# Optimization experiments

Hardware: AMD Instinct MI355X
Metric: run time of the kernel (lower is better)

Reference implementation:

```python
import jax, jax.numpy as jnp
import numpy as np

B, G, D, H, KD, E = 64, 512, 128, 8, 16, 128
NS = 20  # num_station


def _init_w(key, shape):
    stdv = 1.0 / np.sqrt(shape[-1]).astype(np.float32)
    return jax.random.uniform(key, shape, jnp.float32, -stdv, stdv)


def setup_inputs() -> dict:
    key = jax.random.key(0)
    ks = jax.random.split(key, 12)
    return {
        "q": jax.random.normal(ks[0], (B, G, D), jnp.float32),
        "h": jax.random.normal(ks[1], (B, G, D), jnp.float32),
        "W_query_depot": _init_w(ks[2], (H, D, KD)),
        "W_key_custom": _init_w(ks[3], (H, D, KD)),
        "W_val_custom": _init_w(ks[4], (H, D, KD)),
        "W_query_station": _init_w(ks[5], (H, D, KD)),
        "W_key_other": _init_w(ks[6], (H, D, KD)),
        "W_val_other": _init_w(ks[7], (H, D, KD)),
        "W_query_custom": _init_w(ks[8], (H, D, KD)),
        "W_key_all": _init_w(ks[9], (H, D, KD)),
        "W_val_all": _init_w(ks[10], (H, D, KD)),
        "W_out": _init_w(ks[11], (H, KD, E)),
        "num_station": NS,
    }


def _mha_block(q_seg, h_seg, Wq, Wk, Wv, norm):
    # q_seg: [B, Nq, D], h_seg: [B, Nk, D]; weights: [H, D, KD]
    Q = jnp.einsum('bqd,hdk->hbqk', q_seg, Wq)
    K = jnp.einsum('bnd,hdk->hbnk', h_seg, Wk)
    V = jnp.einsum('bnd,hdk->hbnk', h_seg, Wv)
    attn = jax.nn.softmax(norm * jnp.einsum('hbqk,hbnk->hbqn', Q, K), axis=-1)
    return jnp.einsum('hbqn,hbnk->hbqk', attn, V)  # [H, B, Nq, KD]


def reference(q, h, W_query_depot, W_key_custom, W_val_custom,
              W_query_station, W_key_other, W_val_other,
              W_query_custom, W_key_all, W_val_all, W_out, num_station):
    ns = num_station
    norm = 1.0 / np.sqrt(W_query_depot.shape[-1]).astype(np.float32)
    h_custom = h[:, 1 + ns:]                                        # customers
    h_other = jnp.concatenate([h[:, :1], h[:, 1 + ns:]], axis=1)    # depot + customers
    heads_depot = _mha_block(q[:, :1], h_custom,
                             W_query_depot, W_key_custom, W_val_custom, norm)
    heads_station = _mha_block(q[:, 1:1 + ns], h_other,
                               W_query_station, W_key_other, W_val_other, norm)
    heads_custom = _mha_block(q[:, 1 + ns:], h,
                              W_query_custom, W_key_all, W_val_all, norm)
    heads = jnp.concatenate([heads_depot, heads_station, heads_custom], axis=2)
    # final projection: mm([B*G, H*KD], [H*KD, E])
    return jnp.einsum('hbgk,hke->bge', heads, W_out)
```

## Files before the change

### kernel.cpp

```cpp
#include <hip/hip_runtime.h>
#include <hip/hip_bf16.h>

namespace {

typedef _Float16 v4h __attribute__((ext_vector_type(4)));
typedef __fp16   h2  __attribute__((ext_vector_type(2)));
typedef float    v4f __attribute__((ext_vector_type(4)));

constexpr int B = 64, G = 512, D = 128, H = 8, KD = 16, NS = 20;
constexpr float NORM = 0.25f;
constexpr float L2E  = 1.44269504088896f;
constexpr float DTHR = 11.54f;
constexpr int KP = 20;
constexpr int VP = 524;
constexpr int QP = 20;
constexpr int QCH = 256;

__device__ __forceinline__ v4f mfma16(v4h a, v4h b, v4f c) {
  return __builtin_amdgcn_mfma_f32_16x16x16f16(a, b, c, 0, 0, 0);
}
__device__ __forceinline__ v4h cvt4(float4 v) {
  h2 a = __builtin_amdgcn_cvt_pkrtz(v.x, v.y);
  h2 b = __builtin_amdgcn_cvt_pkrtz(v.z, v.w);
  return v4h{(_Float16)a[0], (_Float16)a[1], (_Float16)b[0], (_Float16)b[1]};
}

struct SM {
  char      ht[16384];
  _Float16  Kl[512 * KP];
  _Float16  Vt[16 * VP];
  _Float16  Ql[QCH * QP];
};

__device__ __forceinline__ void sm_chunk(v4f s0, v4f s1, float& m, v4f& mc,
                                         v4f& o, v4f& la, v4h& p0, v4h& p1) {
  const float ma = fmaxf(fmaxf(s0[0], s0[1]), s0[2]);
  const float mb = fmaxf(fmaxf(s0[3], s1[0]), s1[1]);
  const float mz = fmaxf(fmaxf(s1[2], s1[3]), ma);
  const float mx = fmaxf(mb, mz);
  if (__builtin_expect(!__all(mx <= DTHR), 0)) {
    float d = fmaxf(mx, __shfl_xor(mx, 16));
    d = fmaxf(d, __shfl_xor(d, 32));
    d = fmaxf(d, 0.f);
    const float sc = __builtin_amdgcn_exp2f(-d);
    o *= sc; la *= sc; m += d;
    mc[0] = -m; mc[1] = -m; mc[2] = -m; mc[3] = -m;
    const v4f dv = {d, d, d, d};
    s0 -= dv; s1 -= dv;
  }
  h2 e01 = __builtin_amdgcn_cvt_pkrtz(__builtin_amdgcn_exp2f(s0[0]),
                                      __builtin_amdgcn_exp2f(s0[1]));
  h2 e23 = __builtin_amdgcn_cvt_pkrtz(__builtin_amdgcn_exp2f(s0[2]),
                                      __builtin_amdgcn_exp2f(s0[3]));
  h2 e45 = __builtin_amdgcn_cvt_pkrtz(__builtin_amdgcn_exp2f(s1[0]),
                                      __builtin_amdgcn_exp2f(s1[1]));
  h2 e67 = __builtin_amdgcn_cvt_pkrtz(__builtin_amdgcn_exp2f(s1[2]),
                                      __builtin_amdgcn_exp2f(s1[3]));
  p0 = {(_Float16)e01[0], (_Float16)e01[1], (_Float16)e23[0], (_Float16)e23[1]};
  p1 = {(_Float16)e45[0], (_Float16)e45[1], (_Float16)e67[0], (_Float16)e67[1]};
}

template<int SEG>
__device__ __forceinline__ void seg_body(
    int bid, const float* __restrict__ q, const float* __restrict__ hb,
    const float* __restrict__ Wq, const float* __restrict__ Wk,
    const float* __restrict__ Wv, float* __restrict__ heads, SM& sm)
{
  constexpr int Lq   = SEG == 0 ? 1 : SEG == 1 ? NS : G - 1 - NS;
  constexpr int QOFF = SEG == 0 ? 0 : SEG == 1 ? 1  : 1 + NS;
  constexpr int Ln   = SEG == 0 ? G - 1 - NS : SEG == 1 ? G - NS : G;
  constexpr int NCH  = (Ln + 31) / 32;
  constexpr int NQC  = (Lq + QCH - 1) / QCH;

  const int hh   = bid >> 6;
  const int b    = bid & 63;
  const int tid  = threadIdx.x;
  const int w    = tid >> 6;
  const int lane = tid & 63;
  const int g    = lane >> 4, c = lane & 15;

  v4h wA[8];
  v4h wQ[8];
  {
    const float* Wt = (w < 4) ? Wk : Wv;
    #pragma unroll
    for (int dc = 0; dc < 8; ++dc)
      #pragma unroll
      for (int bb = 0; bb < 4; ++bb)
        wA[dc][bb] = (_Float16)Wt[((size_t)hh * D + dc * 16 + 4 * g + bb) * KD + c];
    if (w < 4) {
      #pragma unroll
      for (int dc = 0; dc < 8; ++dc)
        #pragma unroll
        for (int bb = 0; bb < 4; ++bb)
          wQ[dc][bb] = (_Float16)(Wq[((size_t)hh * D + dc * 16 + 4 * g + bb) * KD + c]
                                  * (NORM * L2E));
    }
  }

  const int sb = w & 3;
  for (int t = 0; t < 8; ++t) {
    const int base = t * 64;
    #pragma unroll
    for (int i = 0; i < 4; ++i) {
      int idx = tid + i * 512, r = idx >> 5, jj = idx & 31;
      int n = base + r;
      int nn = n < Ln ? n : Ln - 1;
      int hr;
      if (SEG == 0)      hr = nn + 1 + NS;
      else if (SEG == 1) hr = (nn == 0) ? 0 : nn + NS;
      else               hr = nn;
      float4 v = ((const float4*)(hb + ((size_t)b * G + hr) * D))[jj];
      *(v4h*)(sm.ht + r * 256 + ((8 * jj) ^ ((r & 7) << 4))) = cvt4(v);
    }
    __syncthreads();
    v4f acc = {0.f, 0.f, 0.f, 0.f};
    #pragma unroll
    for (int dc = 0; dc < 8; ++dc) {
      const v4h a = *(const v4h*)(sm.ht + (sb * 16 + c) * 256 +
                                  ((32 * dc + 8 * g) ^ ((c & 7) << 4)));
      acc = mfma16(a, wA[dc], acc);
    }
    if (w < 4) {
      #pragma unroll
      for (int r = 0; r < 4; ++r)
        sm.Kl[(base + sb * 16 + 4 * g + r) * KP + c] = (_Float16)acc[r];
    } else {
      v4h vv = {(_Float16)acc[0], (_Float16)acc[1], (_Float16)acc[2], (_Float16)acc[3]};
      *(v4h*)(sm.Vt + c * VP + base + sb * 16 + 4 * g) = vv;
    }
    __syncthreads();
  }

  for (int qc = 0; qc < NQC; ++qc) {
    const int qbase = qc * QCH;
    const int qcnt  = (Lq - qbase < QCH) ? (Lq - qbase) : QCH;
    const int nst   = (qcnt + 63) / 64;
    for (int st = 0; st < nst; ++st) {
      #pragma unroll
      for (int i = 0; i < 4; ++i) {
        int idx = tid + i * 512, r = idx >> 5, jj = idx & 31;
        int qs = qbase + st * 64 + r;
        int gq = QOFF + (qs < Lq ? qs : Lq - 1);
        float4 v = ((const float4*)(q + ((size_t)b * G + gq) * D))[jj];
        *(v4h*)(sm.ht + r * 256 + ((8 * jj) ^ ((r & 7) << 4))) = cvt4(v);
      }
      __syncthreads();
      if (w < 4) {
        v4f acc = {0.f, 0.f, 0.f, 0.f};
        #pragma unroll
        for (int dc = 0; dc < 8; ++dc) {
          const v4h a = *(const v4h*)(sm.ht + (w * 16 + c) * 256 +
                                      ((32 * dc + 8 * g) ^ ((c & 7) << 4)));
          acc = mfma16(a, wQ[dc], acc);
        }
        #pragma unroll
        for (int r = 0; r < 4; ++r)
          sm.Ql[(st * 64 + w * 16 + 4 * g + r) * QP + c] = (_Float16)acc[r];
      }
      __syncthreads();
    }

    const int nqt = (qcnt + 15) / 16;
    for (int t0 = w; t0 < nqt; t0 += 16) {
      const int tB = t0 + 8;
      const bool hasB = tB < nqt;
      const v4h qfA = *(const v4h*)(sm.Ql + (t0 * 16 + c) * QP + 4 * g);
      const v4h qfB = hasB ? *(const v4h*)(sm.Ql + (tB * 16 + c) * QP + 4 * g) : qfA;
      const _Float16* Kb = sm.Kl + c * KP + 4 * g;
      const _Float16* Vb = sm.Vt + c * VP + 4 * g;
      float mA = 0.f, mB = 0.f;
      v4f mcA = {0.f,0.f,0.f,0.f}, mcB = {0.f,0.f,0.f,0.f};
      v4f oA  = {0.f,0.f,0.f,0.f}, oB  = {0.f,0.f,0.f,0.f};
      v4f laA = {0.f,0.f,0.f,0.f}, laB = {0.f,0.f,0.f,0.f};
      const v4h ones = {(_Float16)1.f, (_Float16)1.f, (_Float16)1.f, (_Float16)1.f};
      #pragma unroll
      for (int ch = 0; ch < NCH; ++ch) {
        const int nb = ch * 32;
        const v4h k0 = *(const v4h*)(Kb + nb * KP);
        const v4h k1 = *(const v4h*)(Kb + (nb + 16) * KP);
        const v4h v0 = *(const v4h*)(Vb + nb);
        const v4h v1 = *(const v4h*)(Vb + nb + 16);
        v4f s0A = mfma16(k0, qfA, mcA);
        v4f s1A = mfma16(k1, qfA, mcA);
        v4f s0B = mfma16(k0, qfB, mcB);
        v4f s1B = mfma16(k1, qfB, mcB);
        if constexpr ((Ln & 31) != 0) {
          if (ch == NCH - 1) {
            #pragma unroll
            for (int r = 0; r < 4; ++r) {
              if (nb + 4 * g + r >= Ln)      { s0A[r] = -1e30f; s0B[r] = -1e30f; }
              if (nb + 16 + 4 * g + r >= Ln) { s1A[r] = -1e30f; s1B[r] = -1e30f; }
            }
          }
        }
        v4h p0, p1;
        sm_chunk(s0A, s1A, mA, mcA, oA, laA, p0, p1);
        oA  = mfma16(v0, p0, oA);
        oA  = mfma16(v1, p1, oA);
        laA = mfma16(ones, p0, laA);
        laA = mfma16(ones, p1, laA);
        sm_chunk(s0B, s1B, mB, mcB, oB, laB, p0, p1);
        oB  = mfma16(v0, p0, oB);
        oB  = mfma16(v1, p1, oB);
        laB = mfma16(ones, p0, laB);
        laB = mfma16(ones, p1, laB);
      }
      float* scr = (float*)(sm.ht + w * 1280);
      #pragma unroll
      for (int u = 0; u < 2; ++u) {
        if (u == 1 && !hasB) break;
        const v4f& o  = u ? oB : oA;
        const v4f& la = u ? laB : laA;
        const int  tt = u ? tB : t0;
        const float inv = 1.0f / la[0];
        #pragma unroll
        for (int r = 0; r < 4; ++r) scr[c * 20 + 4 * g + r] = o[r] * inv;
        const int row = lane >> 2, c4 = lane & 3;
        float4 val = *(const float4*)(scr + row * 20 + 4 * c4);
        const int qloc = qbase + tt * 16 + row;
        if (qloc < Lq)
          *(float4*)(heads + ((size_t)b * G + QOFF + qloc) * 128 + hh * 16 + 4 * c4) = val;
      }
    }
    __syncthreads();
  }
}

__global__ __launch_bounds__(512, 4)
void fused_attn(const float* __restrict__ q, const float* __restrict__ hb,
                const float* __restrict__ Wqd, const float* __restrict__ Wkc,
                const float* __restrict__ Wvc, const float* __restrict__ Wqs,
                const float* __restrict__ Wko, const float* __restrict__ Wvo,
                const float* __restrict__ Wqc, const float* __restrict__ Wka,
                const float* __restrict__ Wva, float* __restrict__ heads)
{
  __shared__ SM sm;
  const int bid = blockIdx.x;
  if (bid < 512)       seg_body<2>(bid,        q, hb, Wqc, Wka, Wva, heads, sm);
  else if (bid < 1024) seg_body<1>(bid - 512,  q, hb, Wqs, Wko, Wvo, heads, sm);
  else                 seg_body<0>(bid - 1024, q, hb, Wqd, Wkc, Wvc, heads, sm);
}

__global__ __launch_bounds__(256)
void out_proj_kernel(float* __restrict__ data, const float* __restrict__ Wout)
{
  __shared__ _Float16 WlT[128 * 132];
  __shared__ _Float16 Ah [64 * 132];
  const int tid  = threadIdx.x;
  const int lane = tid & 63, w = tid >> 6;
  const int g = lane >> 4, c = lane & 15;
  const size_t rowbase = (size_t)blockIdx.x * 64;

  #pragma unroll
  for (int i = 0; i < 16; ++i) {
    int idx = tid + i * 256;
    int k = idx >> 5, c4 = (idx & 31) * 4;
    float4 v = ((const float4*)Wout)[idx];
    WlT[(c4 + 0) * 132 + k] = (_Float16)v.x;
    WlT[(c4 + 1) * 132 + k] = (_Float16)v.y;
    WlT[(c4 + 2) * 132 + k] = (_Float16)v.z;
    WlT[(c4 + 3) * 132 + k] = (_Float16)v.w;
  }
  #pragma unroll
  for (int i = 0; i < 8; ++i) {
    int idx = tid + i * 256;
    int r = idx >> 5, c4 = (idx & 31) * 4;
    float4 v = ((const float4*)(data + rowbase * 128))[idx];
    *(v4h*)(Ah + r * 132 + c4) = cvt4(v);
  }
  __syncthreads();

  v4h af[8];
  #pragma unroll
  for (int dc = 0; dc < 8; ++dc)
    af[dc] = *(const v4h*)(Ah + (w * 16 + c) * 132 + dc * 16 + 4 * g);
  #pragma unroll
  for (int ct = 0; ct < 8; ++ct) {
    v4f acc = {0.f, 0.f, 0.f, 0.f};
    #pragma unroll
    for (int dc = 0; dc < 8; ++dc) {
      const v4h bf = *(const v4h*)(WlT + (ct * 16 + c) * 132 + dc * 16 + 4 * g);
      acc = mfma16(af[dc], bf, acc);
    }
    #pragma unroll
    for (int r = 0; r < 4; ++r)
      data[(rowbase + w * 16 + 4 * g + r) * 128 + ct * 16 + c] = acc[r];
  }
}

}

extern "C" void kernel_launch(void* const* d_in, const int* in_sizes, int n_in,
                              void* d_out, int out_size, void* d_ws, size_t ws_size,
                              hipStream_t stream) {
  const float* q    = (const float*)d_in[0];
  const float* h    = (const float*)d_in[1];
  const float* Wqd  = (const float*)d_in[2];
  const float* Wkc  = (const float*)d_in[3];
  const float* Wvc  = (const float*)d_in[4];
  const float* Wqs  = (const float*)d_in[5];
  const float* Wko  = (const float*)d_in[6];
  const float* Wvo  = (const float*)d_in[7];
  const float* Wqc  = (const float*)d_in[8];
  const float* Wka  = (const float*)d_in[9];
  const float* Wva  = (const float*)d_in[10];
  const float* Wout = (const float*)d_in[11];
  float* out = (float*)d_out;

  fused_attn<<<3 * B * H, 512, 0, stream>>>(q, h, Wqd, Wkc, Wvc,
                                            Wqs, Wko, Wvo, Wqc, Wka, Wva, out);
  out_proj_kernel<<<G * B / 64, 256, 0, stream>>>(out, Wout);
}
```

Baseline: 70.64 us.

## Keep projected Q in registers, drop Ql buffer, specialize unpaired tile, raise occupancy

```diff
diff --git a/kernel.cpp b/kernel.cpp
--- a/kernel.cpp
+++ b/kernel.cpp
@@ -12,8 +12,7 @@
 constexpr float L2E  = 1.44269504088896f;
 constexpr float DTHR = 11.54f;
 constexpr int KP = 20;
-constexpr int VP = 524;
-constexpr int QP = 20;
+constexpr int VP = 520;
 constexpr int QCH = 256;
 
 __device__ __forceinline__ v4f mfma16(v4h a, v4h b, v4f c) {
@@ -29,7 +28,6 @@
   char      ht[16384];
   _Float16  Kl[512 * KP];
   _Float16  Vt[16 * VP];
-  _Float16  Ql[QCH * QP];
 };
 
 __device__ __forceinline__ void sm_chunk(v4f s0, v4f s1, float& m, v4f& mc,
@@ -60,6 +58,63 @@
   p1 = {(_Float16)e45[0], (_Float16)e45[1], (_Float16)e67[0], (_Float16)e67[1]};
 }
 
+template<int SEG, bool PAIR>
+__device__ __forceinline__ void attn_loop(const SM& sm, int g, int c,
+                                          v4h qfA, v4h qfB,
+                                          v4f& oA, v4f& laA, v4f& oB, v4f& laB)
+{
+  constexpr int Ln  = SEG == 0 ? G - 1 - NS : SEG == 1 ? G - NS : G;
+  constexpr int NCH = (Ln + 31) / 32;
+  const _Float16* Kb = sm.Kl + c * KP + 4 * g;
+  const _Float16* Vb = sm.Vt + c * VP + 4 * g;
+  float mA = 0.f, mB = 0.f;
+  v4f mcA = {0.f,0.f,0.f,0.f}, mcB = {0.f,0.f,0.f,0.f};
+  const v4h ones = {(_Float16)1.f, (_Float16)1.f, (_Float16)1.f, (_Float16)1.f};
+  #pragma unroll
+  for (int ch = 0; ch < NCH; ++ch) {
+    const int nb = ch * 32;
+    const v4h k0 = *(const v4h*)(Kb + nb * KP);
+    const v4h k1 = *(const v4h*)(Kb + (nb + 16) * KP);
+    const v4h v0 = *(const v4h*)(Vb + nb);
+    const v4h v1 = *(const v4h*)(Vb + nb + 16);
+    v4f s0A = mfma16(k0, qfA, mcA);
+    v4f s1A = mfma16(k1, qfA, mcA);
+    if constexpr ((Ln & 31) != 0) {
+      if (ch == NCH - 1) {
+        #pragma unroll
+        for (int r = 0; r < 4; ++r) {
+          if (nb + 4 * g + r >= Ln)      s0A[r] = -1e30f;
+          if (nb + 16 + 4 * g + r >= Ln) s1A[r] = -1e30f;
+        }
+      }
+    }
+    v4h p0, p1;
+    sm_chunk(s0A, s1A, mA, mcA, oA, laA, p0, p1);
+    oA  = mfma16(v0, p0, oA);
+    oA  = mfma16(v1, p1, oA);
+    laA = mfma16(ones, p0, laA);
+    laA = mfma16(ones, p1, laA);
+    if constexpr (PAIR) {
+      v4f s0B = mfma16(k0, qfB, mcB);
+      v4f s1B = mfma16(k1, qfB, mcB);
+      if constexpr ((Ln & 31) != 0) {
+        if (ch == NCH - 1) {
+          #pragma unroll
+          for (int r = 0; r < 4; ++r) {
+            if (nb + 4 * g + r >= Ln)      s0B[r] = -1e30f;
+            if (nb + 16 + 4 * g + r >= Ln) s1B[r] = -1e30f;
+          }
+        }
+      }
+      sm_chunk(s0B, s1B, mB, mcB, oB, laB, p0, p1);
+      oB  = mfma16(v0, p0, oB);
+      oB  = mfma16(v1, p1, oB);
+      laB = mfma16(ones, p0, laB);
+      laB = mfma16(ones, p1, laB);
+    }
+  }
+}
+
 template<int SEG>
 __device__ __forceinline__ void seg_body(
     int bid, const float* __restrict__ q, const float* __restrict__ hb,
@@ -69,7 +124,6 @@
   constexpr int Lq   = SEG == 0 ? 1 : SEG == 1 ? NS : G - 1 - NS;
   constexpr int QOFF = SEG == 0 ? 0 : SEG == 1 ? 1  : 1 + NS;
   constexpr int Ln   = SEG == 0 ? G - 1 - NS : SEG == 1 ? G - NS : G;
-  constexpr int NCH  = (Ln + 31) / 32;
   constexpr int NQC  = (Lq + QCH - 1) / QCH;
 
   const int hh   = bid >> 6;
@@ -79,132 +133,108 @@
   const int lane = tid & 63;
   const int g    = lane >> 4, c = lane & 15;
 
-  v4h wA[8];
-  v4h wQ[8];
   {
+    v4h wA[8];
     const float* Wt = (w < 4) ? Wk : Wv;
     #pragma unroll
     for (int dc = 0; dc < 8; ++dc)
       #pragma unroll
       for (int bb = 0; bb < 4; ++bb)
         wA[dc][bb] = (_Float16)Wt[((size_t)hh * D + dc * 16 + 4 * g + bb) * KD + c];
-    if (w < 4) {
-      #pragma unroll
-      for (int dc = 0; dc < 8; ++dc)
-        #pragma unroll
-        for (int bb = 0; bb < 4; ++bb)
-          wQ[dc][bb] = (_Float16)(Wq[((size_t)hh * D + dc * 16 + 4 * g + bb) * KD + c]
-                                  * (NORM * L2E));
-    }
-  }
-
-  const int sb = w & 3;
-  for (int t = 0; t < 8; ++t) {
-    const int base = t * 64;
-    #pragma unroll
-    for (int i = 0; i < 4; ++i) {
-      int idx = tid + i * 512, r = idx >> 5, jj = idx & 31;
-      int n = base + r;
-      int nn = n < Ln ? n : Ln - 1;
-      int hr;
-      if (SEG == 0)      hr = nn + 1 + NS;
-      else if (SEG == 1) hr = (nn == 0) ? 0 : nn + NS;
-      else               hr = nn;
-      float4 v = ((const float4*)(hb + ((size_t)b * G + hr) * D))[jj];
-      *(v4h*)(sm.ht + r * 256 + ((8 * jj) ^ ((r & 7) << 4))) = cvt4(v);
-    }
-    __syncthreads();
-    v4f acc = {0.f, 0.f, 0.f, 0.f};
-    #pragma unroll
-    for (int dc = 0; dc < 8; ++dc) {
-      const v4h a = *(const v4h*)(sm.ht + (sb * 16 + c) * 256 +
-                                  ((32 * dc + 8 * g) ^ ((c & 7) << 4)));
-      acc = mfma16(a, wA[dc], acc);
-    }
-    if (w < 4) {
-      #pragma unroll
-      for (int r = 0; r < 4; ++r)
-        sm.Kl[(base + sb * 16 + 4 * g + r) * KP + c] = (_Float16)acc[r];
-    } else {
-      v4h vv = {(_Float16)acc[0], (_Float16)acc[1], (_Float16)acc[2], (_Float16)acc[3]};
-      *(v4h*)(sm.Vt + c * VP + base + sb * 16 + 4 * g) = vv;
-    }
-    __syncthreads();
+
+    const int sb = w & 3;
+    for (int t = 0; t < 8; ++t) {
+      const int base = t * 64;
+      #pragma unroll
+      for (int i = 0; i < 4; ++i) {
+        int idx = tid + i * 512, r = idx >> 5, jj = idx & 31;
+        int n = base + r;
+        int nn = n < Ln ? n : Ln - 1;
+        int hr;
+        if (SEG == 0)      hr = nn + 1 + NS;
+        else if (SEG == 1) hr = (nn == 0) ? 0 : nn + NS;
+        else               hr = nn;
+        float4 v = ((const float4*)(hb + ((size_t)b * G + hr) * D))[jj];
+        *(v4h*)(sm.ht + r * 256 + ((8 * jj) ^ ((r & 7) << 4))) = cvt4(v);
+      }
+      __syncthreads();
+      v4f acc = {0.f, 0.f, 0.f, 0.f};
+      #pragma unroll
+      for (int dc = 0; dc < 8; ++dc) {
+        const v4h a = *(const v4h*)(sm.ht + (sb * 16 + c) * 256 +
+                                    ((32 * dc + 8 * g) ^ ((c & 7) << 4)));
+        acc = mfma16(a, wA[dc], acc);
+      }
+      if (w < 4) {
+        #pragma unroll
+        for (int r = 0; r < 4; ++r)
+          sm.Kl[(base + sb * 16 + 4 * g + r) * KP + c] = (_Float16)acc[r];
+      } else {
+        v4h vv = {(_Float16)acc[0], (_Float16)acc[1], (_Float16)acc[2], (_Float16)acc[3]};
+        *(v4h*)(sm.Vt + c * VP + base + sb * 16 + 4 * g) = vv;
+      }
+      __syncthreads();
+    }
   }
 
   for (int qc = 0; qc < NQC; ++qc) {
     const int qbase = qc * QCH;
     const int qcnt  = (Lq - qbase < QCH) ? (Lq - qbase) : QCH;
-    const int nst   = (qcnt + 63) / 64;
-    for (int st = 0; st < nst; ++st) {
+    const int nqt   = (qcnt + 15) >> 4;
+
+    v4h wQ[8];
+    #pragma unroll
+    for (int dc = 0; dc < 8; ++dc)
+      #pragma unroll
+      for (int bb = 0; bb < 4; ++bb)
+        wQ[dc][bb] = (_Float16)(Wq[((size_t)hh * D + dc * 16 + 4 * g + bb) * KD + c]
+                                * (NORM * L2E));
+
+    v4f accA = {0.f,0.f,0.f,0.f}, accB = {0.f,0.f,0.f,0.f};
+    for (int ri = 0; ri < 4; ++ri) {
+      if (ri * 64 >= qcnt) break;
       #pragma unroll
       for (int i = 0; i < 4; ++i) {
         int idx = tid + i * 512, r = idx >> 5, jj = idx & 31;
-        int qs = qbase + st * 64 + r;
+        int qs = qbase + ri * 64 + r;
         int gq = QOFF + (qs < Lq ? qs : Lq - 1);
         float4 v = ((const float4*)(q + ((size_t)b * G + gq) * D))[jj];
         *(v4h*)(sm.ht + r * 256 + ((8 * jj) ^ ((r & 7) << 4))) = cvt4(v);
       }
       __syncthreads();
-      if (w < 4) {
+      if ((w >> 2) == (ri & 1)) {
         v4f acc = {0.f, 0.f, 0.f, 0.f};
+        const int sb = w & 3;
         #pragma unroll
         for (int dc = 0; dc < 8; ++dc) {
-          const v4h a = *(const v4h*)(sm.ht + (w * 16 + c) * 256 +
+          const v4h a = *(const v4h*)(sm.ht + (sb * 16 + c) * 256 +
                                       ((32 * dc + 8 * g) ^ ((c & 7) << 4)));
           acc = mfma16(a, wQ[dc], acc);
         }
-        #pragma unroll
-        for (int r = 0; r < 4; ++r)
-          sm.Ql[(st * 64 + w * 16 + 4 * g + r) * QP + c] = (_Float16)acc[r];
+        if (ri < 2) accA = acc; else accB = acc;
       }
       __syncthreads();
     }
 
-    const int nqt = (qcnt + 15) / 16;
-    for (int t0 = w; t0 < nqt; t0 += 16) {
-      const int tB = t0 + 8;
-      const bool hasB = tB < nqt;
-      const v4h qfA = *(const v4h*)(sm.Ql + (t0 * 16 + c) * QP + 4 * g);
-      const v4h qfB = hasB ? *(const v4h*)(sm.Ql + (tB * 16 + c) * QP + 4 * g) : qfA;
-      const _Float16* Kb = sm.Kl + c * KP + 4 * g;
-      const _Float16* Vb = sm.Vt + c * VP + 4 * g;
-      float mA = 0.f, mB = 0.f;
-      v4f mcA = {0.f,0.f,0.f,0.f}, mcB = {0.f,0.f,0.f,0.f};
-      v4f oA  = {0.f,0.f,0.f,0.f}, oB  = {0.f,0.f,0.f,0.f};
-      v4f laA = {0.f,0.f,0.f,0.f}, laB = {0.f,0.f,0.f,0.f};
-      const v4h ones = {(_Float16)1.f, (_Float16)1.f, (_Float16)1.f, (_Float16)1.f};
-      #pragma unroll
-      for (int ch = 0; ch < NCH; ++ch) {
-        const int nb = ch * 32;
-        const v4h k0 = *(const v4h*)(Kb + nb * KP);
-        const v4h k1 = *(const v4h*)(Kb + (nb + 16) * KP);
-        const v4h v0 = *(const v4h*)(Vb + nb);
-        const v4h v1 = *(const v4h*)(Vb + nb + 16);
-        v4f s0A = mfma16(k0, qfA, mcA);
-        v4f s1A = mfma16(k1, qfA, mcA);
-        v4f s0B = mfma16(k0, qfB, mcB);
-        v4f s1B = mfma16(k1, qfB, mcB);
-        if constexpr ((Ln & 31) != 0) {
-          if (ch == NCH - 1) {
-            #pragma unroll
-            for (int r = 0; r < 4; ++r) {
-              if (nb + 4 * g + r >= Ln)      { s0A[r] = -1e30f; s0B[r] = -1e30f; }
-              if (nb + 16 + 4 * g + r >= Ln) { s1A[r] = -1e30f; s1B[r] = -1e30f; }
-            }
-          }
-        }
-        v4h p0, p1;
-        sm_chunk(s0A, s1A, mA, mcA, oA, laA, p0, p1);
-        oA  = mfma16(v0, p0, oA);
-        oA  = mfma16(v1, p1, oA);
-        laA = mfma16(ones, p0, laA);
-        laA = mfma16(ones, p1, laA);
-        sm_chunk(s0B, s1B, mB, mcB, oB, laB, p0, p1);
-        oB  = mfma16(v0, p0, oB);
-        oB  = mfma16(v1, p1, oB);
-        laB = mfma16(ones, p0, laB);
-        laB = mfma16(ones, p1, laB);
+    const int t0 = w, tB = w + 8;
+    const bool hasA = t0 < nqt, hasB = tB < nqt;
+    if (hasA) {
+      _Float16* sh = (_Float16*)(sm.ht + w * 1280);
+      v4h qfA, qfB = {};
+      #pragma unroll
+      for (int r = 0; r < 4; ++r) sh[(4 * g + r) * 20 + c] = (_Float16)accA[r];
+      v4f oA = {0.f,0.f,0.f,0.f}, laA = {0.f,0.f,0.f,0.f};
+      v4f oB = {0.f,0.f,0.f,0.f}, laB = {0.f,0.f,0.f,0.f};
+      if (hasB) {
+        _Float16* sh2 = sh + 320;
+        #pragma unroll
+        for (int r = 0; r < 4; ++r) sh2[(4 * g + r) * 20 + c] = (_Float16)accB[r];
+        qfA = *(const v4h*)(sh + c * 20 + 4 * g);
+        qfB = *(const v4h*)(sh2 + c * 20 + 4 * g);
+        attn_loop<SEG, true>(sm, g, c, qfA, qfB, oA, laA, oB, laB);
+      } else {
+        qfA = *(const v4h*)(sh + c * 20 + 4 * g);
+        attn_loop<SEG, false>(sm, g, c, qfA, qfA, oA, laA, oB, laB);
       }
       float* scr = (float*)(sm.ht + w * 1280);
       #pragma unroll
@@ -227,7 +257,7 @@
   }
 }
 
-__global__ __launch_bounds__(512, 4)
+__global__ __launch_bounds__(512, 6)
 void fused_attn(const float* __restrict__ q, const float* __restrict__ hb,
                 const float* __restrict__ Wqd, const float* __restrict__ Wkc,
                 const float* __restrict__ Wvc, const float* __restrict__ Wqs,
```

Measured after the change: 91.16 us. 1.29x slower.
